# Kernel optimization log

Measured on AMD Instinct MI355X. Metric: run time of the kernel, lower is better.

## Reference

```python
import jax, jax.numpy as jnp
import numpy as np

N, K, C, ECTX, HID = 4096, 48, 128, 384, 512
EPS = 1e-5
SCALE = 30.0

def _gelu(x):
    return jax.nn.gelu(x, approximate=False)

def _layernorm(x, g, b):
    mu = jnp.mean(x, axis=-1, keepdims=True)
    var = jnp.var(x, axis=-1, keepdims=True)
    return (x - mu) * jax.lax.rsqrt(var + EPS) * g + b

def setup_inputs() -> dict:
    key = jax.random.key(0)
    ks = jax.random.split(key, 12)
    d_in = C + ECTX  # 512
    def lin(k, out, inp):
        kw, kb = jax.random.split(k)
        lim = 1.0 / np.sqrt(inp)
        W = jax.random.uniform(kw, (out, inp), jnp.float32, -lim, lim)
        b = jax.random.uniform(kb, (out,), jnp.float32, -lim, lim)
        return W, b
    W_m1, b_m1 = lin(ks[0], C, d_in)   # message MLP: in->width
    W_m2, b_m2 = lin(ks[1], C, C)      # width->width
    W_m3, b_m3 = lin(ks[2], C, C)      # width->out
    W_d1, b_d1 = lin(ks[3], HID, C)    # dense MLP: in->hidden
    W_d2, b_d2 = lin(ks[4], C, HID)    # hidden->out
    return {
        "node_features": jax.random.normal(ks[5], (N, C), jnp.float32),
        "layer_edge_features": jax.random.normal(ks[6], (N, K, ECTX), jnp.float32),
        "mask": jnp.ones((N,), jnp.float32),
        "attention_mask": jnp.ones((N, K), jnp.float32),
        "W_m1": W_m1, "b_m1": b_m1, "W_m2": W_m2, "b_m2": b_m2,
        "W_m3": W_m3, "b_m3": b_m3,
        "g1": jnp.ones((C,), jnp.float32), "beta1": jnp.zeros((C,), jnp.float32),
        "W_d1": W_d1, "b_d1": b_d1, "W_d2": W_d2, "b_d2": b_d2,
        "g2": jnp.ones((C,), jnp.float32), "beta2": jnp.zeros((C,), jnp.float32),
    }

def reference(node_features, layer_edge_features, mask, attention_mask,
              W_m1, b_m1, W_m2, b_m2, W_m3, b_m3, g1, beta1,
              W_d1, b_d1, W_d2, b_d2, g2, beta2):
    # broadcast node features to every neighbor slot and concat edge context: (N, K, C+ECTX)
    h_exp = jnp.broadcast_to(node_features[:, None, :], (N, K, C))
    mlp_in = jnp.concatenate([h_exp, layer_edge_features], axis=-1)
    # per-edge message MLP (depth=2: two hidden gelu layers, linear out)
    h = _gelu(jnp.einsum("nkd,cd->nkc", mlp_in, W_m1) + b_m1)
    h = _gelu(jnp.einsum("nkc,dc->nkd", h, W_m2) + b_m2)
    message = jnp.einsum("nkc,dc->nkd", h, W_m3) + b_m3
    message = attention_mask[:, :, None] * message
    agg = jnp.sum(message, axis=-2) / SCALE            # (N, C)
    x = node_features + agg
    x = _layernorm(x, g1, beta1)
    # dense MLP (depth=1)
    d = _gelu(jnp.einsum("nc,hc->nh", x, W_d1) + b_d1)
    d = jnp.einsum("nh,ch->nc", d, W_d2) + b_d2
    x = x + d
    x = _layernorm(x, g2, beta2)
    return mask[:, None] * x
```

## Files before the change

### kernel.cpp

```cpp
#include <hip/hip_runtime.h>

#define NN 4096
#define KK 48
#define CC 128
#define EC 384
#define DD 512
#define HH 512

typedef short bf16x8 __attribute__((ext_vector_type(8)));
typedef float f32x4 __attribute__((ext_vector_type(4)));

__device__ __forceinline__ unsigned short f2bf(float x){
  union { float f; unsigned int u; } c; c.f = x;
  return (unsigned short)((c.u + 0x7fffu + ((c.u >> 16) & 1u)) >> 16);
}

__device__ __forceinline__ bf16x8 pack8(f32x4 a, f32x4 b){
  bf16x8 r;
  r[0]=(short)f2bf(a[0]); r[1]=(short)f2bf(a[1]);
  r[2]=(short)f2bf(a[2]); r[3]=(short)f2bf(a[3]);
  r[4]=(short)f2bf(b[0]); r[5]=(short)f2bf(b[1]);
  r[6]=(short)f2bf(b[2]); r[7]=(short)f2bf(b[3]);
  return r;
}

__device__ __forceinline__ float gelu_f(float x){
  float s = 1.5957691216057308f * (x + 0.044715f*x*x*x);
  float e = __expf(s);
  float t = 1.0f - 2.0f/(e + 1.0f);
  return 0.5f*x*(1.0f + t);
}

__global__ void cvt_kernel(const float* __restrict__ W1, const float* __restrict__ W2,
                           const float* __restrict__ W3, const float* __restrict__ Wd1,
                           const float* __restrict__ Wd2, unsigned short* __restrict__ o){
  int i = blockIdx.x*256 + threadIdx.x;
  float v;
  if      (i <  65536) v = W1[i];
  else if (i <  81920) v = W2[i-65536];
  else if (i <  98304) v = W3[i-81920];
  else if (i < 163840) v = Wd1[i-98304];
  else                 v = Wd2[i-163840];
  o[i] = f2bf(v);
}

__global__ __launch_bounds__(256, 2) void msg_kernel(
    const float* __restrict__ nodef, const float* __restrict__ edgef,
    const float* __restrict__ attn,
    const unsigned short* __restrict__ W1b, const float* __restrict__ b1,
    const unsigned short* __restrict__ W2b, const float* __restrict__ b2,
    const unsigned short* __restrict__ W3b, const float* __restrict__ b3,
    float* __restrict__ x1)
{
  __shared__ __attribute__((aligned(16))) unsigned short H1[96][136];
  __shared__ __attribute__((aligned(16))) unsigned short H2[96][136];

  const int tid  = threadIdx.x;
  const int lane = tid & 63;
  const int wid  = tid >> 6;
  const int wm   = wid & 1;
  const int wn   = wid >> 1;
  const int l15  = lane & 15;
  const int lg   = lane >> 4;
  const int lg8  = lg*8;
  const int node = blockIdx.x*2 + wm;
  const int colb = wn*64;

  const float* nrow = nodef + (size_t)node*CC;
  const float* erow[3];
  #pragma unroll
  for (int mt=0; mt<3; ++mt)
    erow[mt] = edgef + ((size_t)node*KK + (mt*16 + l15))*EC;

  f32x4 acc[3][4];
  #pragma unroll
  for (int mt=0; mt<3; ++mt)
    #pragma unroll
    for (int nt=0; nt<4; ++nt) acc[mt][nt] = (f32x4){0.f,0.f,0.f,0.f};

  bf16x8 aC[3], bC[4], aN[3], bN[4];
  #pragma unroll
  for (int nt=0; nt<4; ++nt)
    bC[nt] = *(const bf16x8*)(W1b + (size_t)(colb + nt*16 + l15)*DD + lg8);
  #pragma unroll
  for (int mt=0; mt<3; ++mt){
    const float* s = nrow + lg8;
    aC[mt] = pack8(*(const f32x4*)s, *(const f32x4*)(s+4));
  }

  #pragma unroll
  for (int ks=0; ks<16; ++ks){
    if (ks < 15){
      const int k1 = (ks+1)*32;
      #pragma unroll
      for (int nt=0; nt<4; ++nt)
        bN[nt] = *(const bf16x8*)(W1b + (size_t)(colb + nt*16 + l15)*DD + k1 + lg8);
      #pragma unroll
      for (int mt=0; mt<3; ++mt){
        const float* s = (k1 < CC) ? (nrow + k1 + lg8) : (erow[mt] + (k1 - CC) + lg8);
        aN[mt] = pack8(*(const f32x4*)s, *(const f32x4*)(s+4));
      }
    }
    #pragma unroll
    for (int mt=0; mt<3; ++mt)
      #pragma unroll
      for (int nt=0; nt<4; ++nt)
        acc[mt][nt] = __builtin_amdgcn_mfma_f32_16x16x32_bf16(aC[mt], bC[nt], acc[mt][nt], 0,0,0);
    #pragma unroll
    for (int mt=0; mt<3; ++mt) aC[mt] = aN[mt];
    #pragma unroll
    for (int nt=0; nt<4; ++nt) bC[nt] = bN[nt];
  }

  #pragma unroll
  for (int nt=0; nt<4; ++nt){
    const int c = colb + nt*16 + l15;
    const float bb = b1[c];
    #pragma unroll
    for (int mt=0; mt<3; ++mt){
      const int r0 = wm*48 + mt*16 + lg*4;
      #pragma unroll
      for (int j=0; j<4; ++j)
        H1[r0+j][c] = f2bf(gelu_f(acc[mt][nt][j] + bb));
    }
  }
  __syncthreads();

  f32x4 a2[3][4];
  #pragma unroll
  for (int mt=0; mt<3; ++mt)
    #pragma unroll
    for (int nt=0; nt<4; ++nt) a2[mt][nt] = (f32x4){0.f,0.f,0.f,0.f};

  #pragma unroll
  for (int ks=0; ks<4; ++ks){
    const int k0 = ks*32;
    bf16x8 bf_[4], af_[3];
    #pragma unroll
    for (int nt=0; nt<4; ++nt)
      bf_[nt] = *(const bf16x8*)(W2b + (size_t)(colb + nt*16 + l15)*CC + k0 + lg8);
    #pragma unroll
    for (int mt=0; mt<3; ++mt)
      af_[mt] = *(const bf16x8*)&H1[wm*48 + mt*16 + l15][k0 + lg8];
    #pragma unroll
    for (int mt=0; mt<3; ++mt)
      #pragma unroll
      for (int nt=0; nt<4; ++nt)
        a2[mt][nt] = __builtin_amdgcn_mfma_f32_16x16x32_bf16(af_[mt], bf_[nt], a2[mt][nt], 0,0,0);
  }

  #pragma unroll
  for (int nt=0; nt<4; ++nt){
    const int c = colb + nt*16 + l15;
    const float bb = b2[c];
    #pragma unroll
    for (int mt=0; mt<3; ++mt){
      const int r0 = wm*48 + mt*16 + lg*4;
      #pragma unroll
      for (int j=0; j<4; ++j)
        H2[r0+j][c] = f2bf(gelu_f(a2[mt][nt][j] + bb));
    }
  }
  __syncthreads();

  f32x4 a3[3][4];
  #pragma unroll
  for (int mt=0; mt<3; ++mt)
    #pragma unroll
    for (int nt=0; nt<4; ++nt) a3[mt][nt] = (f32x4){0.f,0.f,0.f,0.f};

  #pragma unroll
  for (int ks=0; ks<4; ++ks){
    const int k0 = ks*32;
    bf16x8 bf_[4], af_[3];
    #pragma unroll
    for (int nt=0; nt<4; ++nt)
      bf_[nt] = *(const bf16x8*)(W3b + (size_t)(colb + nt*16 + l15)*CC + k0 + lg8);
    #pragma unroll
    for (int mt=0; mt<3; ++mt)
      af_[mt] = *(const bf16x8*)&H2[wm*48 + mt*16 + l15][k0 + lg8];
    #pragma unroll
    for (int mt=0; mt<3; ++mt)
      #pragma unroll
      for (int nt=0; nt<4; ++nt)
        a3[mt][nt] = __builtin_amdgcn_mfma_f32_16x16x32_bf16(af_[mt], bf_[nt], a3[mt][nt], 0,0,0);
  }

  float av[3][4];
  #pragma unroll
  for (int mt=0; mt<3; ++mt)
    #pragma unroll
    for (int j=0; j<4; ++j)
      av[mt][j] = attn[(size_t)node*KK + mt*16 + lg*4 + j];

  #pragma unroll
  for (int nt=0; nt<4; ++nt){
    const int c = colb + nt*16 + l15;
    const float bb = b3[c];
    float t = 0.f;
    #pragma unroll
    for (int mt=0; mt<3; ++mt)
      #pragma unroll
      for (int j=0; j<4; ++j)
        t += (a3[mt][nt][j] + bb) * av[mt][j];
    t += __shfl_xor(t, 16, 64);
    t += __shfl_xor(t, 32, 64);
    if (lg == 0)
      x1[(size_t)node*CC + c] = nodef[(size_t)node*CC + c] + t*(1.0f/30.0f);
  }
}

__global__ __launch_bounds__(256, 2) void post_kernel(
    const float* __restrict__ x1, const float* __restrict__ mask,
    const float* __restrict__ g1, const float* __restrict__ be1,
    const unsigned short* __restrict__ Wd1b, const float* __restrict__ bd1,
    const unsigned short* __restrict__ Wd2b, const float* __restrict__ bd2,
    const float* __restrict__ g2, const float* __restrict__ be2,
    float* __restrict__ out)
{
  __shared__ __attribute__((aligned(16))) unsigned short xlnB[16][136];
  __shared__ __attribute__((aligned(16))) float          xlnF[16][132];
  __shared__ __attribute__((aligned(16))) unsigned short Hb[16][520];
  __shared__ __attribute__((aligned(16))) float          x2s[16][132];

  const int tid  = threadIdx.x;
  const int lane = tid & 63;
  const int wid  = tid >> 6;
  const int l15  = lane & 15;
  const int lg   = lane >> 4;
  const int lg8  = lg*8;
  const int n0   = blockIdx.x * 16;

  {
    const int nl = tid >> 4;
    const int s  = tid & 15;
    const float* row = x1 + (size_t)(n0+nl)*CC + s*8;
    f32x4 a = *(const f32x4*)row;
    f32x4 b = *(const f32x4*)(row+4);
    float sm = (a[0]+a[1])+(a[2]+a[3]) + (b[0]+b[1])+(b[2]+b[3]);
    float sq = a[0]*a[0]+a[1]*a[1]+a[2]*a[2]+a[3]*a[3]
             + b[0]*b[0]+b[1]*b[1]+b[2]*b[2]+b[3]*b[3];
    sm += __shfl_xor(sm,1,64); sq += __shfl_xor(sq,1,64);
    sm += __shfl_xor(sm,2,64); sq += __shfl_xor(sq,2,64);
    sm += __shfl_xor(sm,4,64); sq += __shfl_xor(sq,4,64);
    sm += __shfl_xor(sm,8,64); sq += __shfl_xor(sq,8,64);
    const float mu = sm*(1.f/128.f);
    const float rs = rsqrtf(sq*(1.f/128.f) - mu*mu + 1e-5f);
    #pragma unroll
    for (int j=0; j<8; ++j){
      const int c = s*8+j;
      float xv = (j<4) ? a[j] : b[j-4];
      float y = (xv-mu)*rs*g1[c] + be1[c];
      xlnF[nl][c] = y;
      xlnB[nl][c] = f2bf(y);
    }
  }
  __syncthreads();

  f32x4 a1[8];
  #pragma unroll
  for (int nt=0; nt<8; ++nt) a1[nt] = (f32x4){0.f,0.f,0.f,0.f};
  #pragma unroll
  for (int ks=0; ks<4; ++ks){
    const int k0 = ks*32;
    bf16x8 af = *(const bf16x8*)&xlnB[l15][k0 + lg8];
    #pragma unroll
    for (int nt=0; nt<8; ++nt){
      const int h = wid*128 + nt*16 + l15;
      bf16x8 bf_ = *(const bf16x8*)(Wd1b + (size_t)h*CC + k0 + lg8);
      a1[nt] = __builtin_amdgcn_mfma_f32_16x16x32_bf16(af, bf_, a1[nt], 0,0,0);
    }
  }
  #pragma unroll
  for (int nt=0; nt<8; ++nt){
    const int h = wid*128 + nt*16 + l15;
    const float bb = bd1[h];
    #pragma unroll
    for (int j=0; j<4; ++j)
      Hb[lg*4+j][h] = f2bf(gelu_f(a1[nt][j] + bb));
  }
  __syncthreads();

  f32x4 a2[2];
  #pragma unroll
  for (int nt=0; nt<2; ++nt) a2[nt] = (f32x4){0.f,0.f,0.f,0.f};
  #pragma unroll
  for (int ks=0; ks<16; ++ks){
    const int k0 = ks*32;
    bf16x8 af = *(const bf16x8*)&Hb[l15][k0 + lg8];
    #pragma unroll
    for (int nt=0; nt<2; ++nt){
      const int c = wid*32 + nt*16 + l15;
      bf16x8 bf_ = *(const bf16x8*)(Wd2b + (size_t)c*HH + k0 + lg8);
      a2[nt] = __builtin_amdgcn_mfma_f32_16x16x32_bf16(af, bf_, a2[nt], 0,0,0);
    }
  }
  #pragma unroll
  for (int nt=0; nt<2; ++nt){
    const int c = wid*32 + nt*16 + l15;
    const float bb = bd2[c];
    #pragma unroll
    for (int j=0; j<4; ++j){
      const int r = lg*4 + j;
      x2s[r][c] = xlnF[r][c] + a2[nt][j] + bb;
    }
  }
  __syncthreads();

  {
    const int nl = tid >> 4;
    const int s  = tid & 15;
    float xv[8];
    float sm = 0.f, sq = 0.f;
    #pragma unroll
    for (int j=0; j<8; ++j){ xv[j] = x2s[nl][s*8+j]; sm += xv[j]; sq += xv[j]*xv[j]; }
    sm += __shfl_xor(sm,1,64); sq += __shfl_xor(sq,1,64);
    sm += __shfl_xor(sm,2,64); sq += __shfl_xor(sq,2,64);
    sm += __shfl_xor(sm,4,64); sq += __shfl_xor(sq,4,64);
    sm += __shfl_xor(sm,8,64); sq += __shfl_xor(sq,8,64);
    const float mu = sm*(1.f/128.f);
    const float rs = rsqrtf(sq*(1.f/128.f) - mu*mu + 1e-5f);
    const float mk = mask[n0+nl];
    f32x4 o0, o1;
    #pragma unroll
    for (int j=0; j<8; ++j){
      const int c = s*8+j;
      float y = (xv[j]-mu)*rs*g2[c] + be2[c];
      if (j < 4) o0[j] = mk*y; else o1[j-4] = mk*y;
    }
    float* orow = out + (size_t)(n0+nl)*CC + s*8;
    *(f32x4*)orow     = o0;
    *(f32x4*)(orow+4) = o1;
  }
}

extern "C" void kernel_launch(void* const* d_in, const int* in_sizes, int n_in,
                              void* d_out, int out_size, void* d_ws, size_t ws_size,
                              hipStream_t stream)
{
  (void)in_sizes; (void)n_in; (void)out_size; (void)ws_size;

  const float* nodef = (const float*)d_in[0];
  const float* edgef = (const float*)d_in[1];
  const float* mask  = (const float*)d_in[2];
  const float* attn  = (const float*)d_in[3];
  const float* W_m1  = (const float*)d_in[4];
  const float* b_m1  = (const float*)d_in[5];
  const float* W_m2  = (const float*)d_in[6];
  const float* b_m2  = (const float*)d_in[7];
  const float* W_m3  = (const float*)d_in[8];
  const float* b_m3  = (const float*)d_in[9];
  const float* g1    = (const float*)d_in[10];
  const float* be1   = (const float*)d_in[11];
  const float* W_d1  = (const float*)d_in[12];
  const float* b_d1  = (const float*)d_in[13];
  const float* W_d2  = (const float*)d_in[14];
  const float* b_d2  = (const float*)d_in[15];
  const float* g2    = (const float*)d_in[16];
  const float* be2   = (const float*)d_in[17];

  unsigned short* wsb  = (unsigned short*)d_ws;
  unsigned short* W1b  = wsb;
  unsigned short* W2b  = wsb + 65536;
  unsigned short* W3b  = wsb + 81920;
  unsigned short* Wd1b = wsb + 98304;
  unsigned short* Wd2b = wsb + 163840;
  float* x1 = (float*)((char*)d_ws + 458752);

  cvt_kernel<<<896, 256, 0, stream>>>(W_m1, W_m2, W_m3, W_d1, W_d2, wsb);
  msg_kernel<<<2048, 256, 0, stream>>>(nodef, edgef, attn,
                                       W1b, b_m1, W2b, b_m2, W3b, b_m3, x1);
  post_kernel<<<256, 256, 0, stream>>>(x1, mask, g1, be1, Wd1b, b_d1,
                                       Wd2b, b_d2, g2, be2, (float*)d_out);
}
```

Before: 539.0 us.

## Precompute node-feature projection once per node and use hardware bf16 packing

The node-feature part of the first message layer is identical for all 48 neighbours, so a new node_kernel computes W1[:, :128]·node + b1 once per node. The message kernel then seeds its accumulators with that result and runs only the 384-wide edge part of the K loop, removing a quarter of the first-layer MFMA work. The change also replaces the software float-to-bf16 rounding with v_cvt_pk_bf16_f32, merges the two LDS buffers into one with an extra barrier, and raises the occupancy hint from 2 to 4. The cost is an extra kernel launch and a small fp32 intermediate round-trip through global memory.

```diff
diff --git a/kernel.cpp b/kernel.cpp
--- a/kernel.cpp
+++ b/kernel.cpp
@@ -10,18 +10,19 @@
 typedef short bf16x8 __attribute__((ext_vector_type(8)));
 typedef float f32x4 __attribute__((ext_vector_type(4)));
 
+__device__ __forceinline__ unsigned int pk2(float lo, float hi){
+  unsigned int r;
+  asm("v_cvt_pk_bf16_f32 %0, %1, %2" : "=v"(r) : "v"(lo), "v"(hi));
+  return r;
+}
 __device__ __forceinline__ unsigned short f2bf(float x){
-  union { float f; unsigned int u; } c; c.f = x;
-  return (unsigned short)((c.u + 0x7fffu + ((c.u >> 16) & 1u)) >> 16);
-}
-
+  return (unsigned short)pk2(x, x);
+}
 __device__ __forceinline__ bf16x8 pack8(f32x4 a, f32x4 b){
-  bf16x8 r;
-  r[0]=(short)f2bf(a[0]); r[1]=(short)f2bf(a[1]);
-  r[2]=(short)f2bf(a[2]); r[3]=(short)f2bf(a[3]);
-  r[4]=(short)f2bf(b[0]); r[5]=(short)f2bf(b[1]);
-  r[6]=(short)f2bf(b[2]); r[7]=(short)f2bf(b[3]);
-  return r;
+  union { unsigned int w[4]; bf16x8 v; } u;
+  u.w[0]=pk2(a[0],a[1]); u.w[1]=pk2(a[2],a[3]);
+  u.w[2]=pk2(b[0],b[1]); u.w[3]=pk2(b[2],b[3]);
+  return u.v;
 }
 
 __device__ __forceinline__ float gelu_f(float x){
@@ -44,16 +45,52 @@
   o[i] = f2bf(v);
 }
 
-__global__ __launch_bounds__(256, 2) void msg_kernel(
+__global__ __launch_bounds__(256, 4) void node_kernel(
+    const float* __restrict__ nodef, const unsigned short* __restrict__ W1b,
+    const float* __restrict__ b1, float* __restrict__ Y)
+{
+  const int tid  = threadIdx.x;
+  const int lane = tid & 63;
+  const int wid  = tid >> 6;
+  const int l15  = lane & 15;
+  const int lg   = lane >> 4;
+  const int lg8  = lg*8;
+  const int rowb = blockIdx.x*64 + wid*16;
+
+  f32x4 acc[8];
+  #pragma unroll
+  for (int nt=0; nt<8; ++nt) acc[nt] = (f32x4){0.f,0.f,0.f,0.f};
+
+  const float* arow = nodef + (size_t)(rowb + l15)*CC;
+  #pragma unroll
+  for (int ks=0; ks<4; ++ks){
+    const int k0 = ks*32;
+    bf16x8 af = pack8(*(const f32x4*)(arow + k0 + lg8), *(const f32x4*)(arow + k0 + lg8 + 4));
+    #pragma unroll
+    for (int nt=0; nt<8; ++nt){
+      bf16x8 bf_ = *(const bf16x8*)(W1b + (size_t)(nt*16 + l15)*DD + k0 + lg8);
+      acc[nt] = __builtin_amdgcn_mfma_f32_16x16x32_bf16(af, bf_, acc[nt], 0,0,0);
+    }
+  }
+  #pragma unroll
+  for (int nt=0; nt<8; ++nt){
+    const int c = nt*16 + l15;
+    const float bb = b1[c];
+    #pragma unroll
+    for (int j=0; j<4; ++j)
+      Y[(size_t)(rowb + lg*4 + j)*CC + c] = acc[nt][j] + bb;
+  }
+}
+
+__global__ __launch_bounds__(256, 4) void msg_kernel(
     const float* __restrict__ nodef, const float* __restrict__ edgef,
-    const float* __restrict__ attn,
-    const unsigned short* __restrict__ W1b, const float* __restrict__ b1,
+    const float* __restrict__ attn, const float* __restrict__ Y,
+    const unsigned short* __restrict__ W1b,
     const unsigned short* __restrict__ W2b, const float* __restrict__ b2,
     const unsigned short* __restrict__ W3b, const float* __restrict__ b3,
     float* __restrict__ x1)
 {
-  __shared__ __attribute__((aligned(16))) unsigned short H1[96][136];
-  __shared__ __attribute__((aligned(16))) unsigned short H2[96][136];
+  __shared__ __attribute__((aligned(16))) unsigned short H[96][136];
 
   const int tid  = threadIdx.x;
   const int lane = tid & 63;
@@ -66,40 +103,42 @@
   const int node = blockIdx.x*2 + wm;
   const int colb = wn*64;
 
-  const float* nrow = nodef + (size_t)node*CC;
   const float* erow[3];
   #pragma unroll
   for (int mt=0; mt<3; ++mt)
     erow[mt] = edgef + ((size_t)node*KK + (mt*16 + l15))*EC;
 
+  float yv[4];
+  #pragma unroll
+  for (int nt=0; nt<4; ++nt)
+    yv[nt] = Y[(size_t)node*CC + colb + nt*16 + l15];
+
   f32x4 acc[3][4];
   #pragma unroll
   for (int mt=0; mt<3; ++mt)
     #pragma unroll
-    for (int nt=0; nt<4; ++nt) acc[mt][nt] = (f32x4){0.f,0.f,0.f,0.f};
+    for (int nt=0; nt<4; ++nt)
+      #pragma unroll
+      for (int j=0; j<4; ++j) acc[mt][nt][j] = yv[nt];
 
   bf16x8 aC[3], bC[4], aN[3], bN[4];
   #pragma unroll
   for (int nt=0; nt<4; ++nt)
-    bC[nt] = *(const bf16x8*)(W1b + (size_t)(colb + nt*16 + l15)*DD + lg8);
-  #pragma unroll
-  for (int mt=0; mt<3; ++mt){
-    const float* s = nrow + lg8;
-    aC[mt] = pack8(*(const f32x4*)s, *(const f32x4*)(s+4));
-  }
-
-  #pragma unroll
-  for (int ks=0; ks<16; ++ks){
-    if (ks < 15){
+    bC[nt] = *(const bf16x8*)(W1b + (size_t)(colb + nt*16 + l15)*DD + CC + lg8);
+  #pragma unroll
+  for (int mt=0; mt<3; ++mt)
+    aC[mt] = pack8(*(const f32x4*)(erow[mt] + lg8), *(const f32x4*)(erow[mt] + lg8 + 4));
+
+  #pragma unroll
+  for (int ks=0; ks<12; ++ks){
+    if (ks < 11){
       const int k1 = (ks+1)*32;
       #pragma unroll
       for (int nt=0; nt<4; ++nt)
-        bN[nt] = *(const bf16x8*)(W1b + (size_t)(colb + nt*16 + l15)*DD + k1 + lg8);
-      #pragma unroll
-      for (int mt=0; mt<3; ++mt){
-        const float* s = (k1 < CC) ? (nrow + k1 + lg8) : (erow[mt] + (k1 - CC) + lg8);
-        aN[mt] = pack8(*(const f32x4*)s, *(const f32x4*)(s+4));
-      }
+        bN[nt] = *(const bf16x8*)(W1b + (size_t)(colb + nt*16 + l15)*DD + CC + k1 + lg8);
+      #pragma unroll
+      for (int mt=0; mt<3; ++mt)
+        aN[mt] = pack8(*(const f32x4*)(erow[mt] + k1 + lg8), *(const f32x4*)(erow[mt] + k1 + lg8 + 4));
     }
     #pragma unroll
     for (int mt=0; mt<3; ++mt)
@@ -115,13 +154,12 @@
   #pragma unroll
   for (int nt=0; nt<4; ++nt){
     const int c = colb + nt*16 + l15;
-    const float bb = b1[c];
     #pragma unroll
     for (int mt=0; mt<3; ++mt){
       const int r0 = wm*48 + mt*16 + lg*4;
       #pragma unroll
       for (int j=0; j<4; ++j)
-        H1[r0+j][c] = f2bf(gelu_f(acc[mt][nt][j] + bb));
+        H[r0+j][c] = f2bf(gelu_f(acc[mt][nt][j]));
     }
   }
   __syncthreads();
@@ -141,13 +179,14 @@
       bf_[nt] = *(const bf16x8*)(W2b + (size_t)(colb + nt*16 + l15)*CC + k0 + lg8);
     #pragma unroll
     for (int mt=0; mt<3; ++mt)
-      af_[mt] = *(const bf16x8*)&H1[wm*48 + mt*16 + l15][k0 + lg8];
+      af_[mt] = *(const bf16x8*)&H[wm*48 + mt*16 + l15][k0 + lg8];
     #pragma unroll
     for (int mt=0; mt<3; ++mt)
       #pragma unroll
       for (int nt=0; nt<4; ++nt)
         a2[mt][nt] = __builtin_amdgcn_mfma_f32_16x16x32_bf16(af_[mt], bf_[nt], a2[mt][nt], 0,0,0);
   }
+  __syncthreads();
 
   #pragma unroll
   for (int nt=0; nt<4; ++nt){
@@ -158,7 +197,7 @@
       const int r0 = wm*48 + mt*16 + lg*4;
       #pragma unroll
       for (int j=0; j<4; ++j)
-        H2[r0+j][c] = f2bf(gelu_f(a2[mt][nt][j] + bb));
+        H[r0+j][c] = f2bf(gelu_f(a2[mt][nt][j] + bb));
     }
   }
   __syncthreads();
@@ -178,7 +217,7 @@
       bf_[nt] = *(const bf16x8*)(W3b + (size_t)(colb + nt*16 + l15)*CC + k0 + lg8);
     #pragma unroll
     for (int mt=0; mt<3; ++mt)
-      af_[mt] = *(const bf16x8*)&H2[wm*48 + mt*16 + l15][k0 + lg8];
+      af_[mt] = *(const bf16x8*)&H[wm*48 + mt*16 + l15][k0 + lg8];
     #pragma unroll
     for (int mt=0; mt<3; ++mt)
       #pragma unroll
@@ -366,10 +405,12 @@
   unsigned short* Wd1b = wsb + 98304;
   unsigned short* Wd2b = wsb + 163840;
   float* x1 = (float*)((char*)d_ws + 458752);
+  float* Y  = (float*)((char*)d_ws + 2555904);
 
   cvt_kernel<<<896, 256, 0, stream>>>(W_m1, W_m2, W_m3, W_d1, W_d2, wsb);
-  msg_kernel<<<2048, 256, 0, stream>>>(nodef, edgef, attn,
-                                       W1b, b_m1, W2b, b_m2, W3b, b_m3, x1);
+  node_kernel<<<64, 256, 0, stream>>>(nodef, W1b, b_m1, Y);
+  msg_kernel<<<2048, 256, 0, stream>>>(nodef, edgef, attn, Y,
+                                       W1b, W2b, b_m2, W3b, b_m3, x1);
   post_kernel<<<256, 256, 0, stream>>>(x1, mask, g1, be1, Wd1b, b_d1,
                                        Wd2b, b_d2, g2, be2, (float*)d_out);
 }
```

Result: no change. 544.9 us (+1.1%).
